# Kernel optimization log

Hardware: AMD Instinct MI355X
Metric: run time of the kernel (lower is better)

## Reference

```python
import jax, jax.numpy as jnp
import numpy as np

N = 50000
E = 800000
IN_C = 128
HID = 32
HEADS = 8
OUT_C = 64
NEG_SLOPE = 0.2


def setup_inputs() -> dict:
    key = jax.random.key(0)
    ks = jax.random.split(key, 12)
    x = jax.random.normal(ks[0], (N, IN_C), dtype=jnp.float32)
    edge_index = jax.random.randint(ks[1], (2, E), 0, N, dtype=jnp.int64)
    s = 0.05
    W1 = jax.random.normal(ks[2], (IN_C, HEADS * HID), dtype=jnp.float32) * s
    a1_src = jax.random.normal(ks[3], (HEADS, HID), dtype=jnp.float32) * s
    a1_dst = jax.random.normal(ks[4], (HEADS, HID), dtype=jnp.float32) * s
    b1 = jnp.zeros((HEADS * HID,), dtype=jnp.float32)
    W2 = jax.random.normal(ks[5], (HEADS * HID, OUT_C), dtype=jnp.float32) * s
    a2_src = jax.random.normal(ks[6], (1, OUT_C), dtype=jnp.float32) * s
    a2_dst = jax.random.normal(ks[7], (1, OUT_C), dtype=jnp.float32) * s
    b2 = jnp.zeros((OUT_C,), dtype=jnp.float32)
    return {"x": x, "edge_index": edge_index, "W1": W1, "a1_src": a1_src,
            "a1_dst": a1_dst, "b1": b1, "W2": W2, "a2_src": a2_src,
            "a2_dst": a2_dst, "b2": b2}


def gat_conv(x, W, a_src, a_dst, bias, src, dst, concat):
    # x: [N, F_in]; W: [F_in, H*C]; a_src/a_dst: [H, C]
    H, C = a_src.shape
    h = (x @ W).reshape(N, H, C)                      # [N, H, C]
    alpha_s = jnp.einsum('nhc,hc->nh', h, a_src)      # [N, H]
    alpha_d = jnp.einsum('nhc,hc->nh', h, a_dst)
    e = alpha_s[src] + alpha_d[dst]                   # [E, H]
    e = jnp.where(e >= 0, e, NEG_SLOPE * e)           # leaky relu
    # segment softmax over destination nodes
    m = jax.ops.segment_max(e, dst, num_segments=N)   # [N, H]
    e = jnp.exp(e - m[dst])
    z = jax.ops.segment_sum(e, dst, num_segments=N)   # [N, H]
    alpha = e / z[dst]                                # [E, H]
    msg = h[src] * alpha[:, :, None]                  # [E, H, C]
    out = jax.ops.segment_sum(msg, dst, num_segments=N)  # [N, H, C]
    if concat:
        out = out.reshape(N, H * C)
    else:
        out = out.mean(axis=1)
    return out + bias


def reference(x, edge_index, W1, a1_src, a1_dst, b1, W2, a2_src, a2_dst, b2):
    src, dst = edge_index[0], edge_index[1]
    # dropout omitted (eval mode)
    h = gat_conv(x, W1, a1_src, a1_dst, b1, src, dst, concat=True)
    h = jax.nn.elu(h)
    out = gat_conv(h, W2, a2_src, a2_dst, b2, src, dst, concat=False)
    return out
```

## Files before the change

### kernel.cpp

```cpp
#include <hip/hip_runtime.h>
#include <cstdint>
#include <cstddef>

#define N_NODES 50000
#define N_EDGES 800000
#define INC 128
#define HID 32
#define HEADS 8
#define OUTC 64
#define F1 (HEADS * HID)
#define NEG 0.2f

typedef unsigned short bf16_t;
typedef __attribute__((ext_vector_type(8))) short bf16x8;
typedef __attribute__((ext_vector_type(4))) float f32x4;

__device__ __forceinline__ float bf2f(bf16_t u) {
  union { unsigned int i; float f; } v;
  v.i = ((unsigned int)u) << 16;
  return v.f;
}
__device__ __forceinline__ bf16_t f2bf(float x) {
  union { float f; unsigned int u; } v;
  v.f = x;
  unsigned int r = v.u + 0x7FFFu + ((v.u >> 16) & 1u);
  return (bf16_t)(r >> 16);
}
__device__ __forceinline__ float lrexp(float v) {
  return expf((v >= 0.f) ? v : NEG * v);
}

__global__ void prep_w(const float* __restrict__ W1, const float* __restrict__ W2,
                       bf16_t* __restrict__ W1t, bf16_t* __restrict__ W2t) {
  int t = blockIdx.x * blockDim.x + threadIdx.x;
  if (t < F1 * INC) {
    int n = t / INC, k = t % INC;
    W1t[t] = f2bf(W1[(size_t)k * F1 + n]);
  } else {
    int u = t - F1 * INC;
    if (u < OUTC * F1) {
      int n = u / F1, k = u % F1;
      W2t[u] = f2bf(W2[(size_t)k * OUTC + n]);
    }
  }
}

template <bool AF32, int HPT, int HTOT>
__global__ __launch_bounds__(256) void mfma_gemm_fused(
    const void* __restrict__ Av, const bf16_t* __restrict__ Bt,
    bf16_t* __restrict__ C, const float* __restrict__ a_src,
    const float* __restrict__ a_dst, float* __restrict__ as,
    float* __restrict__ ad, int M, int N, int K,
    const int* __restrict__ dstE, int* __restrict__ cnt) {
  constexpr int BM = 64, BN = 64, BK = 64;
  __shared__ union SM {
    struct { bf16_t A[BM * BK]; bf16_t B[BN * BK]; } st;
    struct { float ct[64][65]; float pr[64][4]; } epi;
  } sm;

  const int tid = threadIdx.x;

  if (cnt != nullptr) {
    int eid = (blockIdx.y * gridDim.x + blockIdx.x) * 256 + tid;
    if (eid < N_EDGES) atomicAdd(&cnt[dstE[eid]], 1);
  }

  const int wave = tid >> 6, lane = tid & 63;
  const int wm = (wave >> 1) * 32, wn = (wave & 1) * 32;
  const int lr = lane & 15, lq = lane >> 4;
  const int m0 = blockIdx.y * BM, n0 = blockIdx.x * BN;
  const float* A32 = (const float*)Av;
  const bf16_t* A16 = (const bf16_t*)Av;

  f32x4 acc[2][2] = {};

  for (int k0 = 0; k0 < K; k0 += BK) {
#pragma unroll
    for (int p = 0; p < 2; p++) {
      int id = p * 256 + tid;
      int r = id >> 3, c = id & 7;
      int gm = m0 + r;
      uint4 v = make_uint4(0, 0, 0, 0);
      if constexpr (AF32) {
        if (gm < M) {
          const float4* ap =
              reinterpret_cast<const float4*>(&A32[(size_t)gm * K + k0 + c * 8]);
          float4 v0 = ap[0], v1 = ap[1];
          union { bf16_t h[8]; uint4 u; } pk;
          pk.h[0] = f2bf(v0.x); pk.h[1] = f2bf(v0.y);
          pk.h[2] = f2bf(v0.z); pk.h[3] = f2bf(v0.w);
          pk.h[4] = f2bf(v1.x); pk.h[5] = f2bf(v1.y);
          pk.h[6] = f2bf(v1.z); pk.h[7] = f2bf(v1.w);
          v = pk.u;
        }
      } else {
        if (gm < M) v = *reinterpret_cast<const uint4*>(&A16[(size_t)gm * K + k0 + c * 8]);
      }
      *reinterpret_cast<uint4*>(&sm.st.A[r * BK + ((c ^ (r & 7)) * 8)]) = v;
    }
#pragma unroll
    for (int p = 0; p < 2; p++) {
      int id = p * 256 + tid;
      int r = id >> 3, c = id & 7;
      uint4 v = *reinterpret_cast<const uint4*>(&Bt[(size_t)(n0 + r) * K + k0 + c * 8]);
      *reinterpret_cast<uint4*>(&sm.st.B[r * BK + ((c ^ (r & 7)) * 8)]) = v;
    }
    __syncthreads();
#pragma unroll
    for (int kk = 0; kk < 2; kk++) {
      bf16x8 af[2], bfr[2];
#pragma unroll
      for (int mi = 0; mi < 2; mi++) {
        int rr = wm + mi * 16 + lr;
        af[mi] = *reinterpret_cast<const bf16x8*>(
            &sm.st.A[rr * BK + (((kk * 4 + lq) ^ (rr & 7)) * 8)]);
      }
#pragma unroll
      for (int ni = 0; ni < 2; ni++) {
        int rr = wn + ni * 16 + lr;
        bfr[ni] = *reinterpret_cast<const bf16x8*>(
            &sm.st.B[rr * BK + (((kk * 4 + lq) ^ (rr & 7)) * 8)]);
      }
#pragma unroll
      for (int mi = 0; mi < 2; mi++)
#pragma unroll
        for (int ni = 0; ni < 2; ni++)
          acc[mi][ni] = __builtin_amdgcn_mfma_f32_16x16x32_bf16(
              af[mi], bfr[ni], acc[mi][ni], 0, 0, 0);
    }
    __syncthreads();
  }

#pragma unroll
  for (int mi = 0; mi < 2; mi++)
#pragma unroll
    for (int ni = 0; ni < 2; ni++)
#pragma unroll
      for (int r = 0; r < 4; r++)
        sm.epi.ct[wm + mi * 16 + lq * 4 + r][wn + ni * 16 + lr] = acc[mi][ni][r];
  __syncthreads();

#pragma unroll
  for (int mi = 0; mi < 2; mi++)
#pragma unroll
    for (int ni = 0; ni < 2; ni++)
#pragma unroll
      for (int r = 0; r < 4; r++) {
        int gm = m0 + wm + mi * 16 + lq * 4 + r;
        if (gm < M)
          C[(size_t)gm * N + n0 + wn + ni * 16 + lr] = f2bf(acc[mi][ni][r]);
      }

  {
    int row = tid >> 2, part = tid & 3;
    int gn = m0 + row;
    const float* av = ((part & 2) ? a_dst : a_src) + n0 + (part & 1) * 32;
    float dot = 0.f;
#pragma unroll
    for (int c = 0; c < 32; c++) dot += sm.epi.ct[row][(part & 1) * 32 + c] * av[c];
    if constexpr (HPT == 2) {
      if (gn < M) {
        float* tgt = (part & 2) ? ad : as;
        tgt[(size_t)gn * HTOT + (n0 >> 5) + (part & 1)] = dot;
      }
    } else {
      sm.epi.pr[row][part] = dot;
      __syncthreads();
      if (part == 0 && gn < M) {
        as[gn] = sm.epi.pr[row][0] + sm.epi.pr[row][1];
        ad[gn] = sm.epi.pr[row][2] + sm.epi.pr[row][3];
      }
    }
  }
}

__global__ void partial_sum(const int* __restrict__ cnt, int* __restrict__ bsum) {
  __shared__ int s[256];
  int i = blockIdx.x * 256 + threadIdx.x;
  s[threadIdx.x] = (i < N_NODES) ? cnt[i] : 0;
  __syncthreads();
  for (int off = 128; off > 0; off >>= 1) {
    if (threadIdx.x < off) s[threadIdx.x] += s[threadIdx.x + off];
    __syncthreads();
  }
  if (threadIdx.x == 0) bsum[blockIdx.x] = s[0];
}

__global__ void block_scan(const int* __restrict__ cnt, const int* __restrict__ bsum,
                           int* __restrict__ rs, int nb) {
  __shared__ int s[256], sb[256];
  int t = threadIdx.x;
  sb[t] = (t < nb) ? bsum[t] : 0;
  __syncthreads();
  for (int off = 1; off < 256; off <<= 1) {
    int v = (t >= off) ? sb[t - off] : 0;
    __syncthreads();
    sb[t] += v;
    __syncthreads();
  }
  int base = (blockIdx.x > 0) ? sb[blockIdx.x - 1] : 0;
  int i = blockIdx.x * 256 + t;
  int v = (i < N_NODES) ? cnt[i] : 0;
  s[t] = v;
  __syncthreads();
  for (int off = 1; off < 256; off <<= 1) {
    int u = (t >= off) ? s[t - off] : 0;
    __syncthreads();
    s[t] += u;
    __syncthreads();
  }
  if (i < N_NODES) rs[i] = base + s[t] - v;
}

__global__ void fill_csr(const int* __restrict__ src, const int* __restrict__ dst,
                         const int* __restrict__ rs, int* __restrict__ cnt,
                         int* __restrict__ csr_src) {
  int e = blockIdx.x * blockDim.x + threadIdx.x;
  if (e >= N_EDGES) return;
  int d = dst[e];
  int pos = atomicSub(&cnt[d], 1) - 1;
  csr_src[rs[d] + pos] = src[e];
}

__global__ __launch_bounds__(256) void gat_aggr1(
    const int* __restrict__ rs, const int* __restrict__ csr_src,
    const float* __restrict__ as, const float* __restrict__ ad,
    const bf16_t* __restrict__ hb, const float* __restrict__ bias,
    bf16_t* __restrict__ outp) {
  int d = blockIdx.x * 4 + (threadIdx.x >> 6);
  int lane = threadIdx.x & 63;
  if (d >= N_NODES) return;
  int beg = rs[d];
  int end = (d == N_NODES - 1) ? N_EDGES : rs[d + 1];
  const int sh = lane & 7;
  const int ah = lane >> 3;
  float ad_h = ad[(size_t)d * 8 + sh];
  float a0 = 0.f, a1 = 0.f, a2 = 0.f, a3 = 0.f, zacc = 0.f;

  if (beg < end) {
    int ei = beg + (lane >> 3);
    int s_reg = csr_src[(ei < end) ? ei : end - 1];
    float w_reg = (ei < end) ? lrexp(as[(size_t)s_reg * 8 + sh] + ad_h) : 0.f;

    for (int cb = beg; cb < end; cb += 8) {
      const bf16_t* bs[8];
#pragma unroll
      for (int e = 0; e < 8; e++)
        bs[e] = hb + (size_t)__builtin_amdgcn_readlane(s_reg, e << 3) * F1;
      uint2 g[8];
#pragma unroll
      for (int e = 0; e < 8; e++)
        g[e] = *reinterpret_cast<const uint2*>(bs[e] + 4 * lane);
      float w_cur = w_reg;
      zacc += w_reg;
      int nxt = cb + 8;
      if (nxt < end) {
        int ei2 = nxt + (lane >> 3);
        s_reg = csr_src[(ei2 < end) ? ei2 : end - 1];
        w_reg = (ei2 < end) ? lrexp(as[(size_t)s_reg * 8 + sh] + ad_h) : 0.f;
      }
#pragma unroll
      for (int e = 0; e < 8; e++) {
        float wv = __shfl(w_cur, (e << 3) | ah);
        union { uint2 u; bf16_t h[4]; } ld;
        ld.u = g[e];
        a0 += bf2f(ld.h[0]) * wv;
        a1 += bf2f(ld.h[1]) * wv;
        a2 += bf2f(ld.h[2]) * wv;
        a3 += bf2f(ld.h[3]) * wv;
      }
    }
  }

  float zr = zacc;
  zr += __shfl_xor(zr, 8);
  zr += __shfl_xor(zr, 16);
  zr += __shfl_xor(zr, 32);
  float z = __shfl(zr, ah);

  float inv = (end > beg) ? (1.f / z) : 0.f;
  float v0 = a0 * inv + bias[4 * lane + 0];
  float v1 = a1 * inv + bias[4 * lane + 1];
  float v2 = a2 * inv + bias[4 * lane + 2];
  float v3 = a3 * inv + bias[4 * lane + 3];
  v0 = (v0 > 0.f) ? v0 : expm1f(v0);
  v1 = (v1 > 0.f) ? v1 : expm1f(v1);
  v2 = (v2 > 0.f) ? v2 : expm1f(v2);
  v3 = (v3 > 0.f) ? v3 : expm1f(v3);
  union { bf16_t h[4]; uint2 u; } pk;
  pk.h[0] = f2bf(v0); pk.h[1] = f2bf(v1); pk.h[2] = f2bf(v2); pk.h[3] = f2bf(v3);
  *reinterpret_cast<uint2*>(&outp[(size_t)d * F1 + 4 * lane]) = pk.u;
}

__global__ __launch_bounds__(256) void gat_aggr2(
    const int* __restrict__ rs, const int* __restrict__ csr_src,
    const float* __restrict__ as, const float* __restrict__ ad,
    const bf16_t* __restrict__ hb, const float* __restrict__ bias,
    float* __restrict__ outp) {
  int d = blockIdx.x * 32 + (threadIdx.x >> 3);
  int sub = threadIdx.x & 7;
  if (d >= N_NODES) return;
  int beg = rs[d];
  int end = (d == N_NODES - 1) ? N_EDGES : rs[d + 1];
  float ad_d = ad[d];
  float acc[8] = {};
  float zacc = 0.f;

  if (beg < end) {
    int ei = beg + sub;
    int s_reg = csr_src[(ei < end) ? ei : end - 1];
    float w_reg = (ei < end) ? lrexp(as[s_reg] + ad_d) : 0.f;

    for (int cb = beg; cb < end; cb += 8) {
      int sv[8];
#pragma unroll
      for (int e = 0; e < 8; e++) sv[e] = __shfl(s_reg, e, 8);
      uint4 g[8];
#pragma unroll
      for (int e = 0; e < 8; e++)
        g[e] = *reinterpret_cast<const uint4*>(&hb[(size_t)sv[e] * OUTC + 8 * sub]);
      float w_cur = w_reg;
      zacc += w_reg;
      int nxt = cb + 8;
      if (nxt < end) {
        int ei2 = nxt + sub;
        s_reg = csr_src[(ei2 < end) ? ei2 : end - 1];
        w_reg = (ei2 < end) ? lrexp(as[s_reg] + ad_d) : 0.f;
      }
#pragma unroll
      for (int e = 0; e < 8; e++) {
        float wv = __shfl(w_cur, e, 8);
        union { uint4 u; bf16_t h[8]; } ld;
        ld.u = g[e];
#pragma unroll
        for (int q = 0; q < 8; q++) acc[q] += bf2f(ld.h[q]) * wv;
      }
    }
  }

  float zr = zacc;
  zr += __shfl_xor(zr, 1, 8);
  zr += __shfl_xor(zr, 2, 8);
  zr += __shfl_xor(zr, 4, 8);

  float inv = (end > beg) ? (1.f / zr) : 0.f;
  float4 o0, o1;
  o0.x = acc[0] * inv + bias[8 * sub + 0];
  o0.y = acc[1] * inv + bias[8 * sub + 1];
  o0.z = acc[2] * inv + bias[8 * sub + 2];
  o0.w = acc[3] * inv + bias[8 * sub + 3];
  o1.x = acc[4] * inv + bias[8 * sub + 4];
  o1.y = acc[5] * inv + bias[8 * sub + 5];
  o1.z = acc[6] * inv + bias[8 * sub + 6];
  o1.w = acc[7] * inv + bias[8 * sub + 7];
  *reinterpret_cast<float4*>(&outp[(size_t)d * OUTC + 8 * sub]) = o0;
  *reinterpret_cast<float4*>(&outp[(size_t)d * OUTC + 8 * sub + 4]) = o1;
}

extern "C" void kernel_launch(void* const* d_in, const int* in_sizes, int n_in,
                              void* d_out, int out_size, void* d_ws, size_t ws_size,
                              hipStream_t stream) {
  const float* x      = (const float*)d_in[0];
  const int*   ei     = (const int*)d_in[1];
  const float* W1     = (const float*)d_in[2];
  const float* a1_src = (const float*)d_in[3];
  const float* a1_dst = (const float*)d_in[4];
  const float* b1     = (const float*)d_in[5];
  const float* W2     = (const float*)d_in[6];
  const float* a2_src = (const float*)d_in[7];
  const float* a2_dst = (const float*)d_in[8];
  const float* b2     = (const float*)d_in[9];

  const int* src = ei;
  const int* dst = ei + N_EDGES;
  float* out = (float*)d_out;

  char* base = (char*)d_ws;
  size_t off = 0;
  auto carve = [&](size_t bytes) {
    void* q = base + off;
    off += (bytes + 255) & ~size_t(255);
    return q;
  };
  bf16_t* h1b  = (bf16_t*)carve((size_t)N_NODES * F1 * 2);
  bf16_t* o1b  = (bf16_t*)carve((size_t)N_NODES * F1 * 2);
  bf16_t* h2b  = (bf16_t*)carve((size_t)N_NODES * OUTC * 2);
  bf16_t* W1t  = (bf16_t*)carve((size_t)F1 * INC * 2);
  bf16_t* W2t  = (bf16_t*)carve((size_t)OUTC * F1 * 2);
  float* as1 = (float*)carve((size_t)N_NODES * HEADS * 4);
  float* ad1 = (float*)carve((size_t)N_NODES * HEADS * 4);
  float* as2 = (float*)carve((size_t)N_NODES * 4);
  float* ad2 = (float*)carve((size_t)N_NODES * 4);
  int* cnt = (int*)carve((size_t)N_NODES * 4);
  int* rs = (int*)carve((size_t)N_NODES * 4);
  int* bsum = (int*)carve(256 * 4);
  int* csr_src = (int*)carve((size_t)N_EDGES * 4);

  constexpr int NB_SCAN = (N_NODES + 255) / 256;

  hipMemsetAsync(cnt, 0, N_NODES * sizeof(int), stream);

  prep_w<<<(F1 * INC + OUTC * F1 + 255) / 256, 256, 0, stream>>>(W1, W2, W1t, W2t);

  mfma_gemm_fused<true, 2, HEADS><<<dim3(F1 / 64, (N_NODES + 63) / 64), 256, 0, stream>>>(
      x, W1t, h1b, a1_src, a1_dst, as1, ad1, N_NODES, F1, INC, dst, cnt);

  partial_sum<<<NB_SCAN, 256, 0, stream>>>(cnt, bsum);
  block_scan<<<NB_SCAN, 256, 0, stream>>>(cnt, bsum, rs, NB_SCAN);
  fill_csr<<<(N_EDGES + 255) / 256, 256, 0, stream>>>(src, dst, rs, cnt, csr_src);

  gat_aggr1<<<(N_NODES + 3) / 4, 256, 0, stream>>>(rs, csr_src, as1, ad1, h1b, b1, o1b);

  mfma_gemm_fused<false, 1, 1><<<dim3(OUTC / 64, (N_NODES + 63) / 64), 256, 0, stream>>>(
      o1b, W2t, h2b, a2_src, a2_dst, as2, ad2, N_NODES, OUTC, F1, nullptr, nullptr);
  gat_aggr2<<<(N_NODES + 31) / 32, 256, 0, stream>>>(rs, csr_src, as2, ad2, h2b, b2, out);
}
```

Baseline: 291.6 us.

## Merge CSR build into one cooperative kernel, drop weight prep, double-buffer aggregation

Replaces the memset, count, partial-sum, scan and fill kernels with a single cooperative kernel that uses grid syncs, cutting launch overhead. It also removes the separate weight transpose/convert kernel by having the GEMM read fp32 weights and convert them while staging B tiles. Finally, gat_aggr1 double-buffers neighbor row gathers so the next batch of loads is issued before the current batch is accumulated. Risks: strided scalar weight loads in the GEMM, grid.sync cost with only 208 blocks doing atomics, more register pressure in the aggregation, and no longer overlapping the degree count with the first GEMM.

```diff
diff --git a/kernel.cpp b/kernel.cpp
--- a/kernel.cpp
+++ b/kernel.cpp
@@ -1,6 +1,9 @@
 #include <hip/hip_runtime.h>
+#include <hip/hip_cooperative_groups.h>
 #include <cstdint>
 #include <cstddef>
+
+namespace cg = cooperative_groups;
 
 #define N_NODES 50000
 #define N_EDGES 800000
@@ -10,6 +13,7 @@
 #define OUTC 64
 #define F1 (HEADS * HID)
 #define NEG 0.2f
+#define NBLK_CSR 208
 
 typedef unsigned short bf16_t;
 typedef __attribute__((ext_vector_type(8))) short bf16x8;
@@ -30,28 +34,63 @@
   return expf((v >= 0.f) ? v : NEG * v);
 }
 
-__global__ void prep_w(const float* __restrict__ W1, const float* __restrict__ W2,
-                       bf16_t* __restrict__ W1t, bf16_t* __restrict__ W2t) {
-  int t = blockIdx.x * blockDim.x + threadIdx.x;
-  if (t < F1 * INC) {
-    int n = t / INC, k = t % INC;
-    W1t[t] = f2bf(W1[(size_t)k * F1 + n]);
-  } else {
-    int u = t - F1 * INC;
-    if (u < OUTC * F1) {
-      int n = u / F1, k = u % F1;
-      W2t[u] = f2bf(W2[(size_t)k * OUTC + n]);
-    }
+__global__ void csr_build(const int* __restrict__ src, const int* __restrict__ dst,
+                          int* __restrict__ cnt, int* __restrict__ rs,
+                          int* __restrict__ bsum, int* __restrict__ csr_src) {
+  cg::grid_group grid = cg::this_grid();
+  __shared__ int s[256];
+  __shared__ int sb[256];
+  const int t = threadIdx.x, b = blockIdx.x;
+  const int gtid = b * 256 + t;
+  const int gsize = NBLK_CSR * 256;
+  constexpr int NSEG = (N_NODES + 255) / 256;
+
+  for (int i = gtid; i < N_NODES; i += gsize) cnt[i] = 0;
+  grid.sync();
+  for (int e = gtid; e < N_EDGES; e += gsize) atomicAdd(&cnt[dst[e]], 1);
+  grid.sync();
+  if (b < NSEG) {
+    int i = b * 256 + t;
+    int v = (i < N_NODES) ? cnt[i] : 0;
+    s[t] = v;
+    __syncthreads();
+    for (int off = 1; off < 256; off <<= 1) {
+      int u = (t >= off) ? s[t - off] : 0;
+      __syncthreads();
+      s[t] += u;
+      __syncthreads();
+    }
+    if (i < N_NODES) rs[i] = s[t];
+    if (t == 255) bsum[b] = s[255];
+  }
+  grid.sync();
+  if (b < NSEG) {
+    sb[t] = (t < NSEG) ? bsum[t] : 0;
+    __syncthreads();
+    for (int off = 1; off < 256; off <<= 1) {
+      int u = (t >= off) ? sb[t - off] : 0;
+      __syncthreads();
+      sb[t] += u;
+      __syncthreads();
+    }
+    int base = (b > 0) ? sb[b - 1] : 0;
+    int i = b * 256 + t;
+    if (i < N_NODES) rs[i] = base + rs[i] - cnt[i];
+  }
+  grid.sync();
+  for (int e = gtid; e < N_EDGES; e += gsize) {
+    int d = dst[e];
+    int pos = atomicSub(&cnt[d], 1) - 1;
+    csr_src[rs[d] + pos] = src[e];
   }
 }
 
 template <bool AF32, int HPT, int HTOT>
 __global__ __launch_bounds__(256) void mfma_gemm_fused(
-    const void* __restrict__ Av, const bf16_t* __restrict__ Bt,
+    const void* __restrict__ Av, const float* __restrict__ Wf,
     bf16_t* __restrict__ C, const float* __restrict__ a_src,
     const float* __restrict__ a_dst, float* __restrict__ as,
-    float* __restrict__ ad, int M, int N, int K,
-    const int* __restrict__ dstE, int* __restrict__ cnt) {
+    float* __restrict__ ad, int M, int N, int K) {
   constexpr int BM = 64, BN = 64, BK = 64;
   __shared__ union SM {
     struct { bf16_t A[BM * BK]; bf16_t B[BN * BK]; } st;
@@ -59,12 +98,6 @@
   } sm;
 
   const int tid = threadIdx.x;
-
-  if (cnt != nullptr) {
-    int eid = (blockIdx.y * gridDim.x + blockIdx.x) * 256 + tid;
-    if (eid < N_EDGES) atomicAdd(&cnt[dstE[eid]], 1);
-  }
-
   const int wave = tid >> 6, lane = tid & 63;
   const int wm = (wave >> 1) * 32, wn = (wave & 1) * 32;
   const int lr = lane & 15, lq = lane >> 4;
@@ -102,8 +135,11 @@
     for (int p = 0; p < 2; p++) {
       int id = p * 256 + tid;
       int r = id >> 3, c = id & 7;
-      uint4 v = *reinterpret_cast<const uint4*>(&Bt[(size_t)(n0 + r) * K + k0 + c * 8]);
-      *reinterpret_cast<uint4*>(&sm.st.B[r * BK + ((c ^ (r & 7)) * 8)]) = v;
+      union { bf16_t h[8]; uint4 u; } pk;
+#pragma unroll
+      for (int j = 0; j < 8; j++)
+        pk.h[j] = f2bf(Wf[(size_t)(k0 + c * 8 + j) * N + n0 + r]);
+      *reinterpret_cast<uint4*>(&sm.st.B[r * BK + ((c ^ (r & 7)) * 8)]) = pk.u;
     }
     __syncthreads();
 #pragma unroll
@@ -172,54 +208,6 @@
       }
     }
   }
-}
-
-__global__ void partial_sum(const int* __restrict__ cnt, int* __restrict__ bsum) {
-  __shared__ int s[256];
-  int i = blockIdx.x * 256 + threadIdx.x;
-  s[threadIdx.x] = (i < N_NODES) ? cnt[i] : 0;
-  __syncthreads();
-  for (int off = 128; off > 0; off >>= 1) {
-    if (threadIdx.x < off) s[threadIdx.x] += s[threadIdx.x + off];
-    __syncthreads();
-  }
-  if (threadIdx.x == 0) bsum[blockIdx.x] = s[0];
-}
-
-__global__ void block_scan(const int* __restrict__ cnt, const int* __restrict__ bsum,
-                           int* __restrict__ rs, int nb) {
-  __shared__ int s[256], sb[256];
-  int t = threadIdx.x;
-  sb[t] = (t < nb) ? bsum[t] : 0;
-  __syncthreads();
-  for (int off = 1; off < 256; off <<= 1) {
-    int v = (t >= off) ? sb[t - off] : 0;
-    __syncthreads();
-    sb[t] += v;
-    __syncthreads();
-  }
-  int base = (blockIdx.x > 0) ? sb[blockIdx.x - 1] : 0;
-  int i = blockIdx.x * 256 + t;
-  int v = (i < N_NODES) ? cnt[i] : 0;
-  s[t] = v;
-  __syncthreads();
-  for (int off = 1; off < 256; off <<= 1) {
-    int u = (t >= off) ? s[t - off] : 0;
-    __syncthreads();
-    s[t] += u;
-    __syncthreads();
-  }
-  if (i < N_NODES) rs[i] = base + s[t] - v;
-}
-
-__global__ void fill_csr(const int* __restrict__ src, const int* __restrict__ dst,
-                         const int* __restrict__ rs, int* __restrict__ cnt,
-                         int* __restrict__ csr_src) {
-  int e = blockIdx.x * blockDim.x + threadIdx.x;
-  if (e >= N_EDGES) return;
-  int d = dst[e];
-  int pos = atomicSub(&cnt[d], 1) - 1;
-  csr_src[rs[d] + pos] = src[e];
 }
 
 __global__ __launch_bounds__(256) void gat_aggr1(
@@ -233,42 +221,52 @@
   int beg = rs[d];
   int end = (d == N_NODES - 1) ? N_EDGES : rs[d + 1];
   const int sh = lane & 7;
+  const int es = lane >> 3;
   const int ah = lane >> 3;
   float ad_h = ad[(size_t)d * 8 + sh];
   float a0 = 0.f, a1 = 0.f, a2 = 0.f, a3 = 0.f, zacc = 0.f;
 
   if (beg < end) {
-    int ei = beg + (lane >> 3);
-    int s_reg = csr_src[(ei < end) ? ei : end - 1];
-    float w_reg = (ei < end) ? lrexp(as[(size_t)s_reg * 8 + sh] + ad_h) : 0.f;
+    int ei0 = beg + es;
+    int s_cur = csr_src[(ei0 < end) ? ei0 : end - 1];
+    float w_cur = (ei0 < end) ? lrexp(as[(size_t)s_cur * 8 + sh] + ad_h) : 0.f;
+    uint2 g_cur[8];
+#pragma unroll
+    for (int e = 0; e < 8; e++) {
+      const bf16_t* bp =
+          hb + (size_t)__builtin_amdgcn_readlane(s_cur, e << 3) * F1;
+      g_cur[e] = *reinterpret_cast<const uint2*>(bp + 4 * lane);
+    }
+    int ei1 = beg + 8 + es;
+    int s_next = csr_src[(ei1 < end) ? ei1 : end - 1];
+    bool v_next = (ei1 < end);
 
     for (int cb = beg; cb < end; cb += 8) {
-      const bf16_t* bs[8];
-#pragma unroll
-      for (int e = 0; e < 8; e++)
-        bs[e] = hb + (size_t)__builtin_amdgcn_readlane(s_reg, e << 3) * F1;
-      uint2 g[8];
-#pragma unroll
-      for (int e = 0; e < 8; e++)
-        g[e] = *reinterpret_cast<const uint2*>(bs[e] + 4 * lane);
-      float w_cur = w_reg;
-      zacc += w_reg;
-      int nxt = cb + 8;
-      if (nxt < end) {
-        int ei2 = nxt + (lane >> 3);
-        s_reg = csr_src[(ei2 < end) ? ei2 : end - 1];
-        w_reg = (ei2 < end) ? lrexp(as[(size_t)s_reg * 8 + sh] + ad_h) : 0.f;
-      }
+      float w_next = v_next ? lrexp(as[(size_t)s_next * 8 + sh] + ad_h) : 0.f;
+      uint2 g_next[8];
+#pragma unroll
+      for (int e = 0; e < 8; e++) {
+        const bf16_t* bp =
+            hb + (size_t)__builtin_amdgcn_readlane(s_next, e << 3) * F1;
+        g_next[e] = *reinterpret_cast<const uint2*>(bp + 4 * lane);
+      }
+      int ei2 = cb + 16 + es;
+      s_next = csr_src[(ei2 < end) ? ei2 : end - 1];
+      v_next = (ei2 < end);
+      zacc += w_cur;
 #pragma unroll
       for (int e = 0; e < 8; e++) {
         float wv = __shfl(w_cur, (e << 3) | ah);
         union { uint2 u; bf16_t h[4]; } ld;
-        ld.u = g[e];
+        ld.u = g_cur[e];
         a0 += bf2f(ld.h[0]) * wv;
         a1 += bf2f(ld.h[1]) * wv;
         a2 += bf2f(ld.h[2]) * wv;
         a3 += bf2f(ld.h[3]) * wv;
       }
+      w_cur = w_next;
+#pragma unroll
+      for (int e = 0; e < 8; e++) g_cur[e] = g_next[e];
     }
   }
 
@@ -279,10 +277,11 @@
   float z = __shfl(zr, ah);
 
   float inv = (end > beg) ? (1.f / z) : 0.f;
-  float v0 = a0 * inv + bias[4 * lane + 0];
-  float v1 = a1 * inv + bias[4 * lane + 1];
-  float v2 = a2 * inv + bias[4 * lane + 2];
-  float v3 = a3 * inv + bias[4 * lane + 3];
+  float4 bv = *reinterpret_cast<const float4*>(&bias[4 * lane]);
+  float v0 = a0 * inv + bv.x;
+  float v1 = a1 * inv + bv.y;
+  float v2 = a2 * inv + bv.z;
+  float v3 = a3 * inv + bv.w;
   v0 = (v0 > 0.f) ? v0 : expm1f(v0);
   v1 = (v1 > 0.f) ? v1 : expm1f(v1);
   v2 = (v2 > 0.f) ? v2 : expm1f(v2);
@@ -385,8 +384,6 @@
   bf16_t* h1b  = (bf16_t*)carve((size_t)N_NODES * F1 * 2);
   bf16_t* o1b  = (bf16_t*)carve((size_t)N_NODES * F1 * 2);
   bf16_t* h2b  = (bf16_t*)carve((size_t)N_NODES * OUTC * 2);
-  bf16_t* W1t  = (bf16_t*)carve((size_t)F1 * INC * 2);
-  bf16_t* W2t  = (bf16_t*)carve((size_t)OUTC * F1 * 2);
   float* as1 = (float*)carve((size_t)N_NODES * HEADS * 4);
   float* ad1 = (float*)carve((size_t)N_NODES * HEADS * 4);
   float* as2 = (float*)carve((size_t)N_NODES * 4);
@@ -396,22 +393,20 @@
   int* bsum = (int*)carve(256 * 4);
   int* csr_src = (int*)carve((size_t)N_EDGES * 4);
 
-  constexpr int NB_SCAN = (N_NODES + 255) / 256;
-
-  hipMemsetAsync(cnt, 0, N_NODES * sizeof(int), stream);
-
-  prep_w<<<(F1 * INC + OUTC * F1 + 255) / 256, 256, 0, stream>>>(W1, W2, W1t, W2t);
+  {
+    void* cargs[] = {(void*)&src, (void*)&dst, (void*)&cnt,
+                     (void*)&rs,  (void*)&bsum, (void*)&csr_src};
+    hipLaunchCooperativeKernel((void*)csr_build, dim3(NBLK_CSR), dim3(256),
+                               cargs, 0, stream);
+  }
 
   mfma_gemm_fused<true, 2, HEADS><<<dim3(F1 / 64, (N_NODES + 63) / 64), 256, 0, stream>>>(
-      x, W1t, h1b, a1_src, a1_dst, as1, ad1, N_NODES, F1, INC, dst, cnt);
-
-  partial_sum<<<NB_SCAN, 256, 0, stream>>>(cnt, bsum);
-  block_scan<<<NB_SCAN, 256, 0, stream>>>(cnt, bsum, rs, NB_SCAN);
-  fill_csr<<<(N_EDGES + 255) / 256, 256, 0, stream>>>(src, dst, rs, cnt, csr_src);
+      x, W1, h1b, a1_src, a1_dst, as1, ad1, N_NODES, F1, INC);
 
   gat_aggr1<<<(N_NODES + 3) / 4, 256, 0, stream>>>(rs, csr_src, as1, ad1, h1b, b1, o1b);
 
   mfma_gemm_fused<false, 1, 1><<<dim3(OUTC / 64, (N_NODES + 63) / 64), 256, 0, stream>>>(
-      o1b, W2t, h2b, a2_src, a2_dst, as2, ad2, N_NODES, OUTC, F1, nullptr, nullptr);
+      o1b, W2, h2b, a2_src, a2_dst, as2, ad2, N_NODES, OUTC, F1);
+
   gat_aggr2<<<(N_NODES + 31) / 32, 256, 0, stream>>>(rs, csr_src, as2, ad2, h2b, b2, out);
 }
```

After: 416.4 us. 42.8% more time.
